# Kernel tuning notes

Hardware: AMD Instinct MI355X
Metric: run time of the kernel (lower is better)

The kernel has to match this reference:

```python
import jax, jax.numpy as jnp
import numpy as np

LATENT_DIM = 64
NUM_EMBEDDINGS = 16
COMMITMENT_COST = 0.25


def setup_inputs() -> dict:
    key = jax.random.key(0)
    z = jax.random.normal(key, (65536, LATENT_DIM), dtype=jnp.float32)
    # Each per-dimension codebook is initialized to linspace(-1.5, 1.5, K),
    # matching the torch init. Stacked into [latent_dim, num_embeddings].
    row = jnp.linspace(-1.5, 1.5, NUM_EMBEDDINGS, dtype=jnp.float32)
    codebook_w = jnp.broadcast_to(row, (LATENT_DIM, NUM_EMBEDDINGS)).copy()
    return {"z": z, "codebook_w": codebook_w}


def reference(z, codebook_w):
    # z: [B, D]; codebook_w: [D, K] (scalar codebook per latent dim).
    B, D = z.shape
    sg = jax.lax.stop_gradient
    # Squared distances to every code, vectorized over all latent dims: [B, D, K]
    dist = (z[:, :, None] - codebook_w[None, :, :]) ** 2
    indices = jnp.argmin(dist, axis=2)                      # [B, D] int
    # Gather nearest code value per (sample, dim): equivalent to one-hot @ weight
    z_q = codebook_w[jnp.arange(D)[None, :], indices]       # [B, D]
    # commitment: sum over dims of per-dim MSE (mean over batch), z_q detached
    commitment_loss = jnp.sum(jnp.mean((z - sg(z_q)) ** 2, axis=0))
    # codebook loss: mean over all elements, z detached
    codebook_loss = jnp.mean((z_q - sg(z)) ** 2)
    vq_loss = codebook_loss + COMMITMENT_COST * commitment_loss
    # straight-through estimator
    z_q_sg = z + sg(z_q - z)
    return (z_q_sg, vq_loss, indices)
```

## Files before the change

kernel.cpp:

```cpp
#include <hip/hip_runtime.h>

constexpr int B_SZ = 65536;
constexpr int D_SZ = 64;
constexpr int K_SZ = 16;
constexpr int N_ELEM = B_SZ * D_SZ;
constexpr int N_VEC  = N_ELEM / 4;
constexpr int NBLOCKS  = 1024;
constexpr int NTHREADS = 256;
constexpr float LOSS_SCALE = 4.0531158447265625e-06f;

__global__ __launch_bounds__(NTHREADS, 4)
void vq_main(const float* __restrict__ z, const float* __restrict__ cb,
             float* __restrict__ zq, float* __restrict__ idx,
             float* __restrict__ partials)
{
    const int t    = threadIdx.x;
    const int gtid = blockIdx.x * NTHREADS + t;
    const int stride = NBLOCKS * NTHREADS;
    const int d0 = 4 * (gtid & 15);

    float c[4][K_SZ];
#pragma unroll
    for (int j = 0; j < 4; ++j) {
        const float4* row = (const float4*)(cb + (d0 + j) * K_SZ);
#pragma unroll
        for (int q = 0; q < 4; ++q) {
            float4 r = row[q];
            c[j][4*q+0] = r.x; c[j][4*q+1] = r.y;
            c[j][4*q+2] = r.z; c[j][4*q+3] = r.w;
        }
    }

    float local = 0.0f;
    for (int v = gtid; v < N_VEC; v += stride) {
        float4 zv = ((const float4*)z)[v];
        float zs[4] = {zv.x, zv.y, zv.z, zv.w};
        float qv[4], kf[4];
#pragma unroll
        for (int j = 0; j < 4; ++j) {
            float diff = zs[j] - c[j][0];
            float best = diff * diff;
            float bc = c[j][0];
            int bk = 0;
#pragma unroll
            for (int k = 1; k < K_SZ; ++k) {
                float dk = zs[j] - c[j][k];
                float dist = dk * dk;
                if (dist < best) { best = dist; bk = k; bc = c[j][k]; }
            }
            qv[j] = bc;
            kf[j] = (float)bk;
            local += best;
        }
        ((float4*)zq)[v] = make_float4(qv[0], qv[1], qv[2], qv[3]);
        const int e = 4 * v;
        idx[e+0] = kf[0]; idx[e+1] = kf[1]; idx[e+2] = kf[2]; idx[e+3] = kf[3];
    }

#pragma unroll
    for (int off = 32; off > 0; off >>= 1)
        local += __shfl_down(local, off, 64);
    __shared__ float s[NTHREADS / 64];
    if ((t & 63) == 0) s[t >> 6] = local;
    __syncthreads();
    if (t == 0) {
        float bsum = 0.f;
#pragma unroll
        for (int w = 0; w < NTHREADS / 64; ++w) bsum += s[w];
        partials[blockIdx.x] = bsum;
    }
}

__global__ __launch_bounds__(256)
void vq_reduce(const float* __restrict__ partials, float* __restrict__ loss)
{
    const int t = threadIdx.x;
    float local = 0.0f;
    for (int i = t; i < NBLOCKS; i += 256) local += partials[i];
#pragma unroll
    for (int off = 32; off > 0; off >>= 1)
        local += __shfl_down(local, off, 64);
    __shared__ float s[4];
    if ((t & 63) == 0) s[t >> 6] = local;
    __syncthreads();
    if (t == 0) loss[0] = (s[0] + s[1] + s[2] + s[3]) * LOSS_SCALE;
}

extern "C" void kernel_launch(void* const* d_in, const int* in_sizes, int n_in,
                              void* d_out, int out_size, void* d_ws, size_t ws_size,
                              hipStream_t stream)
{
    const float* z  = (const float*)d_in[0];
    const float* cb = (const float*)d_in[1];
    float* out  = (float*)d_out;
    float* zq   = out;
    float* loss = out + N_ELEM;
    float* idx  = out + N_ELEM + 1;
    float* partials = (float*)d_ws;

    vq_main<<<NBLOCKS, NTHREADS, 0, stream>>>(z, cb, zq, idx, partials);
    vq_reduce<<<1, 256, 0, stream>>>(partials, loss);
}
```

Before: 89.64 us.

## Map lanes to latent dims with scalar coalesced nontemporal loads, one pass per thread

Each lane now owns one latent dimension, so it keeps a 16-entry codebook row instead of four rows, which cuts register pressure. Each thread handles exactly four elements with no grid-stride loop, using 4096 blocks. All z loads and zq/idx stores are per-element, fully coalesced, and nontemporal. This replaces the float4 z/zq accesses and the unaligned scalar idx stores. The trade-off is scalar 4-byte accesses instead of 16-byte ones and more blocks feeding the partial-sum reduction.

```diff
diff --git a/kernel.cpp b/kernel.cpp
--- a/kernel.cpp
+++ b/kernel.cpp
@@ -4,57 +4,49 @@
 constexpr int D_SZ = 64;
 constexpr int K_SZ = 16;
 constexpr int N_ELEM = B_SZ * D_SZ;
-constexpr int N_VEC  = N_ELEM / 4;
-constexpr int NBLOCKS  = 1024;
+constexpr int NBLOCKS  = 4096;
 constexpr int NTHREADS = 256;
 constexpr float LOSS_SCALE = 4.0531158447265625e-06f;
 
-__global__ __launch_bounds__(NTHREADS, 4)
+__global__ __launch_bounds__(NTHREADS)
 void vq_main(const float* __restrict__ z, const float* __restrict__ cb,
              float* __restrict__ zq, float* __restrict__ idx,
              float* __restrict__ partials)
 {
     const int t    = threadIdx.x;
-    const int gtid = blockIdx.x * NTHREADS + t;
-    const int stride = NBLOCKS * NTHREADS;
-    const int d0 = 4 * (gtid & 15);
+    const int lane = t & 63;
+    const int wave_base = blockIdx.x * 1024 + (t >> 6) * 256;
 
-    float c[4][K_SZ];
+    float c[K_SZ];
+    const float4* crow = (const float4*)(cb + lane * K_SZ);
+#pragma unroll
+    for (int q = 0; q < 4; ++q) {
+        float4 r = crow[q];
+        c[4*q+0] = r.x; c[4*q+1] = r.y; c[4*q+2] = r.z; c[4*q+3] = r.w;
+    }
+
+    float zs[4];
+#pragma unroll
+    for (int j = 0; j < 4; ++j)
+        zs[j] = __builtin_nontemporal_load(z + wave_base + j * 64 + lane);
+
+    float local = 0.0f;
 #pragma unroll
     for (int j = 0; j < 4; ++j) {
-        const float4* row = (const float4*)(cb + (d0 + j) * K_SZ);
+        const int e = wave_base + j * 64 + lane;
+        float diff = zs[j] - c[0];
+        float best = diff * diff;
+        float bc   = c[0];
+        int   bk   = 0;
 #pragma unroll
-        for (int q = 0; q < 4; ++q) {
-            float4 r = row[q];
-            c[j][4*q+0] = r.x; c[j][4*q+1] = r.y;
-            c[j][4*q+2] = r.z; c[j][4*q+3] = r.w;
+        for (int k = 1; k < K_SZ; ++k) {
+            float dk   = zs[j] - c[k];
+            float dist = dk * dk;
+            if (dist < best) { best = dist; bk = k; bc = c[k]; }
         }
-    }
-
-    float local = 0.0f;
-    for (int v = gtid; v < N_VEC; v += stride) {
-        float4 zv = ((const float4*)z)[v];
-        float zs[4] = {zv.x, zv.y, zv.z, zv.w};
-        float qv[4], kf[4];
-#pragma unroll
-        for (int j = 0; j < 4; ++j) {
-            float diff = zs[j] - c[j][0];
-            float best = diff * diff;
-            float bc = c[j][0];
-            int bk = 0;
-#pragma unroll
-            for (int k = 1; k < K_SZ; ++k) {
-                float dk = zs[j] - c[j][k];
-                float dist = dk * dk;
-                if (dist < best) { best = dist; bk = k; bc = c[j][k]; }
-            }
-            qv[j] = bc;
-            kf[j] = (float)bk;
-            local += best;
-        }
-        ((float4*)zq)[v] = make_float4(qv[0], qv[1], qv[2], qv[3]);
-        const int e = 4 * v;
-        idx[e+0] = kf[0]; idx[e+1] = kf[1]; idx[e+2] = kf[2]; idx[e+3] = kf[3];
+        local += best;
+        __builtin_nontemporal_store(bc, zq + e);
+        __builtin_nontemporal_store((float)bk, idx + e);
     }
 
 #pragma unroll
@@ -76,7 +68,9 @@
 {
     const int t = threadIdx.x;
     float local = 0.0f;
-    for (int i = t; i < NBLOCKS; i += 256) local += partials[i];
+#pragma unroll
+    for (int i = 0; i < NBLOCKS / 256; ++i)
+        local += partials[i * 256 + t];
 #pragma unroll
     for (int off = 32; off > 0; off >>= 1)
         local += __shfl_down(local, off, 64);
```

New measurement: 84.04 us. 1.07x faster.
